# Kernel optimization log

Measured on AMD Instinct MI355X. Metric: run time of the kernel, lower is better.

## Reference

```python
import jax, jax.numpy as jnp
import numpy as np

N, E, D, H = 100000, 800000, 128, 4
DK = D // H
SCALE = 1.0 / np.sqrt(D)  # keep logits tame with random weights
EPS = 1e-5


def _layernorm(x, g, b):
    mu = jnp.mean(x, axis=-1, keepdims=True)
    var = jnp.mean(jnp.square(x - mu), axis=-1, keepdims=True)
    return (x - mu) * jax.lax.rsqrt(var + EPS) * g + b


def setup_inputs() -> dict:
    key = jax.random.key(0)
    ks = jax.random.split(key, 14)
    inp = {
        'h': jax.random.normal(ks[0], (N, D), jnp.float32),
        'e_ij': jax.random.normal(ks[1], (E, D), jnp.float32),
        'W1': jax.random.normal(ks[2], (D, D), jnp.float32) * SCALE,
        'W2': jax.random.normal(ks[3], (D, D), jnp.float32) * SCALE,
        'W3': jax.random.normal(ks[4], (D, D), jnp.float32) * SCALE,
        'W4': jax.random.normal(ks[5], (D, D), jnp.float32) * SCALE,
        'W5': jax.random.normal(ks[6], (D, D), jnp.float32) * SCALE,
        'W6': jax.random.normal(ks[7], (D, D), jnp.float32) * SCALE,
        'ln_gamma': jnp.ones((D,), jnp.float32),
        'ln_beta': jnp.zeros((D,), jnp.float32),
        'mlp_w1': jax.random.normal(ks[8], (D, 2 * D), jnp.float32) * SCALE,
        'mlp_w2': jax.random.normal(ks[9], (2 * D, D), jnp.float32) * (1.0 / np.sqrt(2 * D)),
        'src': jax.random.randint(ks[10], (E,), 0, N, jnp.int32),
        'dst': jax.random.randint(ks[11], (E,), 0, N, jnp.int32),
    }
    return inp


def reference(h, e_ij, W1, W2, W3, W4, W5, W6, ln_gamma, ln_beta, mlp_w1, mlp_w2, src, dst):
    u = (h @ W1).reshape(N, H, DK)      # src-side query
    v = (h @ W2).reshape(N, H, DK)      # dst-side
    x3 = (e_ij @ W3).reshape(E, H, DK)
    # m = v[dst] + x_ij ; attn = u[src] * m (elementwise per head/channel)
    m = v[dst] + x3                      # [E,H,DK]
    attn = (u[src] * m) / np.sqrt(DK)    # [E,H,DK]
    # edge_softmax: segment softmax over incoming edges of each dst node
    amax = jax.ops.segment_max(attn, dst, num_segments=N)   # [N,H,DK]
    ex = jnp.exp(attn - amax[dst])
    denom = jax.ops.segment_sum(ex, dst, num_segments=N)    # [N,H,DK]
    alpha = ex / denom[dst]
    k = (h @ W4).reshape(N, H, DK)
    x5 = (e_ij @ W5).reshape(E, H, DK)
    m2 = k[dst] + x5                     # [E,H,DK]
    agg = jax.ops.segment_sum(alpha * m2, dst, num_segments=N).reshape(N, D)
    h1 = h @ W6 + agg
    h1 = _layernorm(h1, ln_gamma, ln_beta)
    mlp_out = jax.nn.relu(h1 @ mlp_w1) @ mlp_w2
    h2 = _layernorm(h1 + mlp_out, ln_gamma, ln_beta)  # same LayerNorm params reused
    return h2
```

## Files before the change

### kernel.cpp

```cpp
#include <hip/hip_runtime.h>
#include <hip/hip_bf16.h>

#define N_NODES 100000
#define N_EDGES 800000

typedef __attribute__((ext_vector_type(8))) short short8v;
typedef __attribute__((ext_vector_type(4))) float f32x4;

__device__ __forceinline__ unsigned short f2bf(float f) {
    __hip_bfloat16 b = __float2bfloat16(f);
    return *(unsigned short*)&b;
}
__device__ __forceinline__ float bf2f(unsigned short u) {
    return __uint_as_float((unsigned)u << 16);
}
__device__ __forceinline__ unsigned pack2(float lo, float hi) {
    return (unsigned)f2bf(lo) | ((unsigned)f2bf(hi) << 16);
}

__device__ __forceinline__ void gload_lds16(const void* g, void* l) {
    __builtin_amdgcn_global_load_lds(
        (const __attribute__((address_space(1))) unsigned int*)g,
        (__attribute__((address_space(3))) unsigned int*)l,
        16, 0, 0);
}

__device__ __forceinline__ int xcd_swizzle(int orig, int q, int r) {
    int xcd = orig & 7, loc = orig >> 3;
    return (xcd < r ? xcd * (q + 1) : r * (q + 1) + (xcd - r) * q) + loc;
}

__global__ __launch_bounds__(256) void hist_dst(
    const int* __restrict__ dst, int* __restrict__ counts)
{
    int e = blockIdx.x * 256 + threadIdx.x;
    if (e < N_EDGES) atomicAdd(&counts[dst[e]], 1);
}

__global__ __launch_bounds__(256) void scan_p1(
    const int* __restrict__ in, int* __restrict__ partials, int n)
{
    __shared__ int ws[4];
    int t = threadIdx.x, lane = t & 63, wv = t >> 6;
    int base = blockIdx.x * 1024;
    int s = 0;
#pragma unroll
    for (int i = 0; i < 4; ++i) {
        int idx = base + i * 256 + t;
        s += (idx < n) ? in[idx] : 0;
    }
#pragma unroll
    for (int off = 1; off < 64; off <<= 1) s += __shfl_xor(s, off);
    if (lane == 0) ws[wv] = s;
    __syncthreads();
    if (t == 0) partials[blockIdx.x] = ws[0] + ws[1] + ws[2] + ws[3];
}

__global__ __launch_bounds__(64) void scan_p2(
    int* __restrict__ partials, int nb, int* __restrict__ total_out)
{
    int lane = threadIdx.x;
    int carry = 0;
    for (int base = 0; base < nb; base += 64) {
        int idx = base + lane;
        int v = (idx < nb) ? partials[idx] : 0;
        int s = v;
#pragma unroll
        for (int off = 1; off < 64; off <<= 1) {
            int w = __shfl_up(s, off);
            if (lane >= off) s += w;
        }
        if (idx < nb) partials[idx] = s - v + carry;
        carry += __shfl(s, 63);
    }
    if (lane == 0) *total_out = carry;
}

__global__ __launch_bounds__(256) void scan_p3(
    const int* __restrict__ in, int* __restrict__ out, int* __restrict__ cursor,
    const int* __restrict__ partials, int n)
{
    __shared__ int ws[4];
    __shared__ int wpre[4];
    __shared__ int s_tot;
    int t = threadIdx.x, lane = t & 63, wv = t >> 6;
    int base = blockIdx.x * 1024;
    int carry = partials[blockIdx.x];
    for (int sub = 0; sub < 4; ++sub) {
        int idx = base + sub * 256 + t;
        int v = (idx < n) ? in[idx] : 0;
        int s = v;
#pragma unroll
        for (int off = 1; off < 64; off <<= 1) {
            int w = __shfl_up(s, off);
            if (lane >= off) s += w;
        }
        if (lane == 63) ws[wv] = s;
        __syncthreads();
        if (t == 0) {
            int a = 0;
#pragma unroll
            for (int i = 0; i < 4; ++i) { wpre[i] = a; a += ws[i]; }
            s_tot = a;
        }
        __syncthreads();
        int excl = s - v + wpre[wv] + carry;
        if (idx < n) { out[idx] = excl; if (cursor) cursor[idx] = excl; }
        carry += s_tot;
        __syncthreads();
    }
}

__global__ __launch_bounds__(256) void scatter_edges(
    const int* __restrict__ dst, const int* __restrict__ src,
    int* __restrict__ cursor,
    int* __restrict__ edge_ord, int* __restrict__ src_ord,
    int* __restrict__ dst_ord)
{
    int e = blockIdx.x * 256 + threadIdx.x;
    if (e < N_EDGES) {
        int d = dst[e];
        int pos = atomicAdd(&cursor[d], 1);
        edge_ord[pos] = e;
        src_ord[pos] = src[e];
        dst_ord[pos] = d;
    }
}

__global__ __launch_bounds__(256) void calc_npieces(
    const int* __restrict__ offsets, int* __restrict__ npieces)
{
    int n = blockIdx.x * 256 + threadIdx.x;
    if (n < N_NODES) {
        int b = offsets[n], e = offsets[n + 1];
        npieces[n] = (e > b) ? (((e - 1) >> 6) - (b >> 6) + 1) : 0;
    }
}

__global__ __launch_bounds__(256) void prep_weights(
    const float* __restrict__ W1, const float* __restrict__ W2,
    const float* __restrict__ W3, const float* __restrict__ W4,
    const float* __restrict__ W5, const float* __restrict__ W6,
    const float* __restrict__ mw1, const float* __restrict__ mw2,
    unsigned short* __restrict__ w3t, unsigned short* __restrict__ w5t,
    unsigned short* __restrict__ wcatt,
    unsigned short* __restrict__ mw1t, unsigned short* __restrict__ mw2t)
{
    int bid = blockIdx.x;
    if (bid < 64) {
        int t = bid * 256 + threadIdx.x;
        int r = t >> 7, c = t & 127;
        w3t[c * 128 + r] = f2bf(W3[t]);
        w5t[c * 128 + r] = f2bf(W5[t]);
    } else if (bid < 320) {
        int t = (bid - 64) * 256 + threadIdx.x;
        int n = t >> 7, k = t & 127;
        const float* Wm = (n < 128) ? W1 : (n < 256) ? W2 : (n < 384) ? W4 : W6;
        wcatt[t] = f2bf(Wm[k * 128 + (n & 127)]);
    } else {
        int t = (bid - 320) * 256 + threadIdx.x;
        if (t < 32768) {
            int n = t >> 7, k = t & 127;
            mw1t[t] = f2bf(mw1[k * 256 + n]);
        } else {
            int s = t - 32768;
            int n = s >> 8, k = s & 255;
            mw2t[s] = f2bf(mw2[k * 128 + n]);
        }
    }
}

__global__ __launch_bounds__(256) void gemm_node(
    const float* __restrict__ A, const unsigned short* __restrict__ Bt,
    unsigned short* __restrict__ uvkb, float* __restrict__ hw6f)
{
    const int t = threadIdx.x;
    const int lane = t & 63, wv = t >> 6;
    const int l15 = lane & 15, kg = lane >> 4;
    const int m0 = blockIdx.x * 64;
    const int n0 = blockIdx.y * 128;
    const int M = N_NODES, K = 128;

    int arow = m0 + wv * 16 + l15;
    int arow_c = arow < M ? arow : M - 1;
    const float* ap = A + (size_t)arow_c * K + kg * 8;

    f32x4 acc[8];
#pragma unroll
    for (int nt = 0; nt < 8; ++nt) acc[nt] = (f32x4){0.f, 0.f, 0.f, 0.f};

    for (int ko = 0; ko < K; ko += 32) {
        float4 f0 = *(const float4*)(ap + ko);
        float4 f1 = *(const float4*)(ap + ko + 4);
        short8v af;
        af[0] = (short)f2bf(f0.x); af[1] = (short)f2bf(f0.y);
        af[2] = (short)f2bf(f0.z); af[3] = (short)f2bf(f0.w);
        af[4] = (short)f2bf(f1.x); af[5] = (short)f2bf(f1.y);
        af[6] = (short)f2bf(f1.z); af[7] = (short)f2bf(f1.w);
#pragma unroll
        for (int nt = 0; nt < 8; ++nt) {
            short8v bf = *(const short8v*)(Bt + (size_t)(n0 + nt * 16 + l15) * K + ko + kg * 8);
            acc[nt] = __builtin_amdgcn_mfma_f32_16x16x32_bf16(af, bf, acc[nt], 0, 0, 0);
        }
    }
#pragma unroll
    for (int nt = 0; nt < 8; ++nt) {
#pragma unroll
        for (int r = 0; r < 4; ++r) {
            int row = m0 + wv * 16 + kg * 4 + r;
            if (row < M) {
                int col = n0 + nt * 16 + l15;
                float vfl = acc[nt][r];
                if (n0 < 384) uvkb[(size_t)row * 384 + col] = f2bf(vfl);
                else          hw6f[(size_t)row * 128 + col - 384] = vfl;
            }
        }
    }
}

__global__ __launch_bounds__(256, 4) void edge_agg(
    const float* __restrict__ e_ij,
    const unsigned short* __restrict__ w3t, const unsigned short* __restrict__ w5t,
    const unsigned short* __restrict__ uvkb,
    const int* __restrict__ edge_ord, const int* __restrict__ src_ord,
    const int* __restrict__ dst_ord,
    const int* __restrict__ offsets, const int* __restrict__ ppos,
    float* __restrict__ dpart, float* __restrict__ apart)
{
    __shared__ __align__(16) float e_s[64 * 128];
    __shared__ int s_eid[64], s_src[64], s_dst[64];
    __shared__ int s_sb[64], s_se[64], s_pi[64];
    __shared__ int s_nseg;

    const int t  = threadIdx.x;
    const int lane = t & 63, wv = t >> 6;
    const int l15 = lane & 15, kg = lane >> 4;
    const int cb = wv * 32 + 2 * l15;
    const float inv = 0.17677669529663687f;

    const int nwg = N_EDGES / 64;
    const int bswz = xcd_swizzle((int)blockIdx.x, nwg >> 3, nwg & 7);
    const int e0 = bswz * 64;

    if (t < 64) {
        s_eid[t] = edge_ord[e0 + t];
        s_src[t] = src_ord[e0 + t];
        int d = dst_ord[e0 + t];
        s_dst[t] = d;
        int dprev = __shfl_up(d, 1);
        bool bnd = (t == 0) || (d != dprev);
        unsigned long long mask = __ballot(bnd);
        int sid = __popcll(mask & ((1ull << t) - 1ull));
        if (bnd) {
            s_sb[sid] = t;
            s_pi[sid] = ppos[d] + bswz - (offsets[d] >> 6);
            if (t > 0) s_se[sid - 1] = t;
        }
        if (t == 63) {
            int ns = __popcll(mask);
            s_se[ns - 1] = 64;
            s_nseg = ns;
        }
    }
    __syncthreads();

#pragma unroll
    for (int i = 0; i < 8; ++i) {
        int c = i * 256 + t;
        int row = c >> 5, j = c & 31;
        int js = j ^ (row & 7);
        const float* g = e_ij + (size_t)s_eid[row] * 128 + js * 4;
        void* l = (void*)((char*)(&e_s[0]) + (size_t)i * 4096 + (size_t)wv * 1024);
        gload_lds16(g, l);
    }
    __syncthreads();

    unsigned short* eb = (unsigned short*)&e_s[0];
    {
        const int crow = t >> 2, q = t & 3;
        float4 fr[8];
#pragma unroll
        for (int i = 0; i < 8; ++i) {
            int j = (q * 8 + i) ^ (crow & 7);
            fr[i] = *(const float4*)(&e_s[crow * 128 + j * 4]);
        }
        __syncthreads();
#pragma unroll
        for (int i = 0; i < 4; ++i) {
            short8v pk;
            pk[0] = (short)f2bf(fr[2 * i].x);     pk[1] = (short)f2bf(fr[2 * i].y);
            pk[2] = (short)f2bf(fr[2 * i].z);     pk[3] = (short)f2bf(fr[2 * i].w);
            pk[4] = (short)f2bf(fr[2 * i + 1].x); pk[5] = (short)f2bf(fr[2 * i + 1].y);
            pk[6] = (short)f2bf(fr[2 * i + 1].z); pk[7] = (short)f2bf(fr[2 * i + 1].w);
            int c = (q * 4 + i) ^ (crow & 15);
            *(short8v*)(eb + crow * 128 + c * 8) = pk;
        }
    }
    __syncthreads();

    const int nseg = __builtin_amdgcn_readfirstlane(s_nseg);

    f32x4 a3[4][2], a5[4][2];
#pragma unroll
    for (int m = 0; m < 4; ++m) {
        a3[m][0] = (f32x4){0.f, 0.f, 0.f, 0.f};
        a3[m][1] = (f32x4){0.f, 0.f, 0.f, 0.f};
        a5[m][0] = (f32x4){0.f, 0.f, 0.f, 0.f};
        a5[m][1] = (f32x4){0.f, 0.f, 0.f, 0.f};
    }
    {
        const unsigned short* b3p0 = w3t + (size_t)(cb + 0) * 128 + kg * 8;
        const unsigned short* b3p1 = w3t + (size_t)(cb + 1) * 128 + kg * 8;
        const unsigned short* b5p0 = w5t + (size_t)(cb + 0) * 128 + kg * 8;
        const unsigned short* b5p1 = w5t + (size_t)(cb + 1) * 128 + kg * 8;
#pragma unroll
        for (int kidx = 0; kidx < 4; ++kidx) {
            const int ko = kidx * 32;
            short8v b30 = *(const short8v*)(b3p0 + ko);
            short8v b31 = *(const short8v*)(b3p1 + ko);
            short8v b50 = *(const short8v*)(b5p0 + ko);
            short8v b51 = *(const short8v*)(b5p1 + ko);
#pragma unroll
            for (int m = 0; m < 4; ++m) {
                const int row = m * 16 + l15;
                short8v af = *(const short8v*)(eb + row * 128 + (((kidx << 2) | kg) ^ l15) * 8);
                a3[m][0] = __builtin_amdgcn_mfma_f32_16x16x32_bf16(af, b30, a3[m][0], 0, 0, 0);
                a3[m][1] = __builtin_amdgcn_mfma_f32_16x16x32_bf16(af, b31, a3[m][1], 0, 0, 0);
                a5[m][0] = __builtin_amdgcn_mfma_f32_16x16x32_bf16(af, b50, a5[m][0], 0, 0, 0);
                a5[m][1] = __builtin_amdgcn_mfma_f32_16x16x32_bf16(af, b51, a5[m][1], 0, 0, 0);
            }
        }
    }

#pragma unroll
    for (int m = 0; m < 4; ++m) {
#pragma unroll
        for (int r = 0; r < 4; ++r) {
            int le = m * 16 + kg * 4 + r;
            int d  = s_dst[le];
            int sv = s_src[le];
            unsigned upk = *(const unsigned*)&uvkb[(size_t)sv * 384 + cb];
            unsigned vpk = *(const unsigned*)&uvkb[(size_t)d * 384 + 128 + cb];
            float u0 = bf2f((unsigned short)(upk & 0xffffu));
            float u1 = bf2f((unsigned short)(upk >> 16));
            float v0 = bf2f((unsigned short)(vpk & 0xffffu));
            float v1 = bf2f((unsigned short)(vpk >> 16));
            float at0 = u0 * (v0 + a3[m][0][r]) * inv;
            float at1 = u1 * (v1 + a3[m][1][r]) * inv;
            float ex0 = __expf(fminf(at0, 80.f));
            float ex1 = __expf(fminf(at1, 80.f));
            a3[m][0][r] = ex0;
            a3[m][1][r] = ex1;
            a5[m][0][r] = ex0 * a5[m][0][r];
            a5[m][1][r] = ex1 * a5[m][1][r];
        }
    }

    for (int sg = 0; sg < nseg; ++sg) {
        const int b  = __builtin_amdgcn_readfirstlane(s_sb[sg]);
        const int e2 = __builtin_amdgcn_readfirstlane(s_se[sg]);
        const int pi = __builtin_amdgcn_readfirstlane(s_pi[sg]);
        float d0 = 0.f, d1 = 0.f, g0 = 0.f, g1 = 0.f;
#pragma unroll
        for (int m = 0; m < 4; ++m) {
            if (b < m * 16 + 16 && e2 > m * 16) {
#pragma unroll
                for (int r = 0; r < 4; ++r) {
                    int slot = m * 16 + kg * 4 + r;
                    bool in = (slot >= b) && (slot < e2);
                    d0 += in ? a3[m][0][r] : 0.f;
                    d1 += in ? a3[m][1][r] : 0.f;
                    g0 += in ? a5[m][0][r] : 0.f;
                    g1 += in ? a5[m][1][r] : 0.f;
                }
            }
        }
        d0 += __shfl_xor(d0, 16); d0 += __shfl_xor(d0, 32);
        d1 += __shfl_xor(d1, 16); d1 += __shfl_xor(d1, 32);
        g0 += __shfl_xor(g0, 16); g0 += __shfl_xor(g0, 32);
        g1 += __shfl_xor(g1, 16); g1 += __shfl_xor(g1, 32);
        if (kg == 0) {
            *(float2*)&dpart[(size_t)pi * 128 + cb] = make_float2(d0, d1);
            *(float2*)&apart[(size_t)pi * 128 + cb] = make_float2(g0, g1);
        }
    }
}

__global__ __launch_bounds__(256, 2) void node_tail(
    const float* __restrict__ hw6f, const unsigned short* __restrict__ uvkb,
    const float* __restrict__ dpart, const float* __restrict__ apart,
    const int* __restrict__ ppos,
    const unsigned short* __restrict__ mw1t, const unsigned short* __restrict__ mw2t,
    const float* __restrict__ gamma, const float* __restrict__ beta,
    float* __restrict__ out)
{
    __shared__ __align__(16) float h1f[64 * 132];
    __shared__ __align__(16) unsigned short hid[64 * 264];

    const int t = threadIdx.x;
    const int lane = t & 63, wv = t >> 6;
    const int l15 = lane & 15, kg = lane >> 4;
    const int nb = blockIdx.x * 64;

    for (int i = 0; i < 16; ++i) {
        int row = wv * 16 + i;
        int n = nb + row;
        int nc = n < N_NODES ? n : N_NODES - 1;
        int p0 = ppos[nc], p1 = ppos[nc + 1];
        float de0 = 0.f, de1 = 0.f, g0 = 0.f, g1 = 0.f;
        for (int j = p0; j < p1; ++j) {
            float2 dv = *(const float2*)&dpart[(size_t)j * 128 + lane * 2];
            float2 av = *(const float2*)&apart[(size_t)j * 128 + lane * 2];
            de0 += dv.x; de1 += dv.y;
            g0  += av.x; g1  += av.y;
        }
        unsigned kpk = *(const unsigned*)&uvkb[(size_t)nc * 384 + 256 + lane * 2];
        float k0 = bf2f((unsigned short)(kpk & 0xffffu));
        float k1 = bf2f((unsigned short)(kpk >> 16));
        float2 hw = *(const float2*)&hw6f[(size_t)nc * 128 + lane * 2];
        float x0 = hw.x + (de0 > 0.f ? k0 + g0 / de0 : 0.f);
        float x1 = hw.y + (de1 > 0.f ? k1 + g1 / de1 : 0.f);
        float s = x0 + x1;
#pragma unroll
        for (int off = 1; off < 64; off <<= 1) s += __shfl_xor(s, off);
        float mu = s * (1.f / 128.f);
        float d0 = x0 - mu, d1 = x1 - mu;
        float ss = d0 * d0 + d1 * d1;
#pragma unroll
        for (int off = 1; off < 64; off <<= 1) ss += __shfl_xor(ss, off);
        float rs = rsqrtf(ss * (1.f / 128.f) + 1e-5f);
        float2 g = *(const float2*)&gamma[lane * 2];
        float2 b = *(const float2*)&beta[lane * 2];
        h1f[row * 132 + lane * 2]     = d0 * rs * g.x + b.x;
        h1f[row * 132 + lane * 2 + 1] = d1 * rs * g.y + b.y;
    }
    __syncthreads();

    {
        const int arow = wv * 16 + l15;
        f32x4 acc[16];
#pragma unroll
        for (int nt = 0; nt < 16; ++nt) acc[nt] = (f32x4){0.f, 0.f, 0.f, 0.f};
#pragma unroll
        for (int kidx = 0; kidx < 4; ++kidx) {
            const int ko = kidx * 32;
            const float* rp = &h1f[arow * 132 + ko + kg * 8];
            float4 f0 = *(const float4*)rp;
            float4 f1 = *(const float4*)(rp + 4);
            short8v af;
            af[0] = (short)f2bf(f0.x); af[1] = (short)f2bf(f0.y);
            af[2] = (short)f2bf(f0.z); af[3] = (short)f2bf(f0.w);
            af[4] = (short)f2bf(f1.x); af[5] = (short)f2bf(f1.y);
            af[6] = (short)f2bf(f1.z); af[7] = (short)f2bf(f1.w);
#pragma unroll
            for (int nt = 0; nt < 16; ++nt) {
                short8v bf = *(const short8v*)(mw1t + (size_t)(nt * 16 + l15) * 128 + ko + kg * 8);
                acc[nt] = __builtin_amdgcn_mfma_f32_16x16x32_bf16(af, bf, acc[nt], 0, 0, 0);
            }
        }
#pragma unroll
        for (int nt = 0; nt < 16; ++nt) {
#pragma unroll
            for (int r = 0; r < 4; ++r) {
                int row = wv * 16 + kg * 4 + r;
                int col = nt * 16 + l15;
                hid[row * 264 + col] = f2bf(fmaxf(acc[nt][r], 0.f));
            }
        }
    }
    __syncthreads();

    {
        const int arow = wv * 16 + l15;
        f32x4 acc[8];
#pragma unroll
        for (int nt = 0; nt < 8; ++nt) acc[nt] = (f32x4){0.f, 0.f, 0.f, 0.f};
#pragma unroll
        for (int kidx = 0; kidx < 8; ++kidx) {
            const int ko = kidx * 32;
            short8v af = *(const short8v*)&hid[arow * 264 + ko + kg * 8];
#pragma unroll
            for (int nt = 0; nt < 8; ++nt) {
                short8v bf = *(const short8v*)(mw2t + (size_t)(nt * 16 + l15) * 256 + ko + kg * 8);
                acc[nt] = __builtin_amdgcn_mfma_f32_16x16x32_bf16(af, bf, acc[nt], 0, 0, 0);
            }
        }
        float gv[8], bv[8];
#pragma unroll
        for (int nt = 0; nt < 8; ++nt) {
            gv[nt] = gamma[nt * 16 + l15];
            bv[nt] = beta[nt * 16 + l15];
        }
#pragma unroll
        for (int r = 0; r < 4; ++r) {
            int lrow = wv * 16 + kg * 4 + r;
            int grow = nb + lrow;
            float x[8];
            float s = 0.f;
#pragma unroll
            for (int nt = 0; nt < 8; ++nt) {
                x[nt] = acc[nt][r] + h1f[lrow * 132 + nt * 16 + l15];
                s += x[nt];
            }
#pragma unroll
            for (int off = 1; off < 16; off <<= 1) s += __shfl_xor(s, off);
            float mu = s * (1.f / 128.f);
            float ss = 0.f;
#pragma unroll
            for (int nt = 0; nt < 8; ++nt) {
                float d = x[nt] - mu;
                ss += d * d;
            }
#pragma unroll
            for (int off = 1; off < 16; off <<= 1) ss += __shfl_xor(ss, off);
            float rsv = rsqrtf(ss * (1.f / 128.f) + 1e-5f);
            if (grow < N_NODES) {
#pragma unroll
                for (int nt = 0; nt < 8; ++nt)
                    out[(size_t)grow * 128 + nt * 16 + l15] =
                        (x[nt] - mu) * rsv * gv[nt] + bv[nt];
            }
        }
    }
}

extern "C" void kernel_launch(void* const* d_in, const int* in_sizes, int n_in,
                              void* d_out, int out_size, void* d_ws, size_t ws_size,
                              hipStream_t stream)
{
    const float* h    = (const float*)d_in[0];
    const float* e_ij = (const float*)d_in[1];
    const float* W1   = (const float*)d_in[2];
    const float* W2   = (const float*)d_in[3];
    const float* W3   = (const float*)d_in[4];
    const float* W4   = (const float*)d_in[5];
    const float* W5   = (const float*)d_in[6];
    const float* W6   = (const float*)d_in[7];
    const float* ln_g = (const float*)d_in[8];
    const float* ln_b = (const float*)d_in[9];
    const float* mw1  = (const float*)d_in[10];
    const float* mw2  = (const float*)d_in[11];
    const int*   src  = (const int*)d_in[12];
    const int*   dst  = (const int*)d_in[13];
    float* out = (float*)d_out;

    float* ws = (float*)d_ws;
    float* hw6f  = ws;
    float* dpart = ws + 25600000;
    float* apart = ws + 40100000;
    unsigned short* uvkb  = (unsigned short*)(ws + 54600000);
    unsigned short* w3t   = (unsigned short*)(ws + 93000000);
    unsigned short* w5t   = w3t + 16384;
    unsigned short* wcatt = w5t + 16384;
    unsigned short* mw1t  = wcatt + 65536;
    unsigned short* mw2t  = mw1t + 32768;
    int* ibase    = (int*)(ws + 93100000);
    int* counts   = ibase;
    int* offsets  = ibase + 100000;
    int* cursor   = ibase + 200001;
    int* npieces  = ibase + 300001;
    int* ppos     = ibase + 400001;
    int* partials = ibase + 500102;
    int* edge_ord = ibase + 500230;
    int* src_ord  = edge_ord + N_EDGES;
    int* dst_ord  = src_ord + N_EDGES;

    dim3 blk(256);
    hipMemsetAsync(counts, 0, N_NODES * sizeof(int), stream);

    hist_dst<<<N_EDGES / 256, blk, 0, stream>>>(dst, counts);
    scan_p1<<<98, blk, 0, stream>>>(counts, partials, N_NODES);
    scan_p2<<<1, 64, 0, stream>>>(partials, 98, offsets + N_NODES);
    scan_p3<<<98, blk, 0, stream>>>(counts, offsets, cursor, partials, N_NODES);
    scatter_edges<<<N_EDGES / 256, blk, 0, stream>>>(dst, src, cursor,
                                                     edge_ord, src_ord, dst_ord);
    calc_npieces<<<391, blk, 0, stream>>>(offsets, npieces);
    scan_p1<<<98, blk, 0, stream>>>(npieces, partials, N_NODES);
    scan_p2<<<1, 64, 0, stream>>>(partials, 98, ppos + N_NODES);
    scan_p3<<<98, blk, 0, stream>>>(npieces, ppos, (int*)nullptr, partials, N_NODES);

    prep_weights<<<576, blk, 0, stream>>>(W1, W2, W3, W4, W5, W6, mw1, mw2,
                                          w3t, w5t, wcatt, mw1t, mw2t);

    gemm_node<<<dim3(1563, 4), blk, 0, stream>>>(h, wcatt, uvkb, hw6f);

    edge_agg<<<N_EDGES / 64, blk, 0, stream>>>(e_ij, w3t, w5t, uvkb,
                                               edge_ord, src_ord, dst_ord,
                                               offsets, ppos, dpart, apart);

    node_tail<<<1563, blk, 0, stream>>>(hw6f, uvkb, dpart, apart, ppos,
                                        mw1t, mw2t, ln_g, ln_b, out);
}
```

Measured before the change: 672.7 us.

## Split node tail into per-node finalize kernel and separate MLP kernel

The fused node_tail kernel, which reduced edge partials, applied the first LayerNorm and ran the MLP with the second LayerNorm, is split in two. node_finalize assigns one wavefront per node and writes h1 in fp32 and bf16 to workspace. mlp_tail reads the bf16 h1 as its MFMA A operand and the fp32 h1 as the residual, and asks for higher occupancy. The aim is more parallelism in the serial, latency-bound partial reduction, which looped over 16 nodes per wave. The cost is an extra launch and an extra round trip of h1 through global memory.

```diff
diff --git a/kernel.cpp b/kernel.cpp
--- a/kernel.cpp
+++ b/kernel.cpp
@@ -386,72 +386,73 @@
     }
 }
 
-__global__ __launch_bounds__(256, 2) void node_tail(
+__global__ __launch_bounds__(256) void node_finalize(
     const float* __restrict__ hw6f, const unsigned short* __restrict__ uvkb,
     const float* __restrict__ dpart, const float* __restrict__ apart,
     const int* __restrict__ ppos,
+    const float* __restrict__ gamma, const float* __restrict__ beta,
+    float* __restrict__ h1, unsigned short* __restrict__ h1b)
+{
+    int n = blockIdx.x * 4 + (threadIdx.x >> 6);
+    int lane = threadIdx.x & 63;
+    int p0 = ppos[n], p1 = ppos[n + 1];
+    float de0 = 0.f, de1 = 0.f, g0 = 0.f, g1 = 0.f;
+    for (int j = p0; j < p1; ++j) {
+        float2 dv = *(const float2*)&dpart[(size_t)j * 128 + lane * 2];
+        float2 av = *(const float2*)&apart[(size_t)j * 128 + lane * 2];
+        de0 += dv.x; de1 += dv.y;
+        g0  += av.x; g1  += av.y;
+    }
+    unsigned kpk = *(const unsigned*)&uvkb[(size_t)n * 384 + 256 + lane * 2];
+    float k0 = bf2f((unsigned short)(kpk & 0xffffu));
+    float k1 = bf2f((unsigned short)(kpk >> 16));
+    float2 hw = *(const float2*)&hw6f[(size_t)n * 128 + lane * 2];
+    float x0 = hw.x + (de0 > 0.f ? k0 + g0 / de0 : 0.f);
+    float x1 = hw.y + (de1 > 0.f ? k1 + g1 / de1 : 0.f);
+    float s = x0 + x1;
+#pragma unroll
+    for (int off = 1; off < 64; off <<= 1) s += __shfl_xor(s, off);
+    float mu = s * (1.f / 128.f);
+    float d0 = x0 - mu, d1 = x1 - mu;
+    float ss = d0 * d0 + d1 * d1;
+#pragma unroll
+    for (int off = 1; off < 64; off <<= 1) ss += __shfl_xor(ss, off);
+    float rs = rsqrtf(ss * (1.f / 128.f) + 1e-5f);
+    float2 g = *(const float2*)&gamma[lane * 2];
+    float2 b = *(const float2*)&beta[lane * 2];
+    float o0 = d0 * rs * g.x + b.x;
+    float o1 = d1 * rs * g.y + b.y;
+    size_t base = (size_t)n * 128 + lane * 2;
+    *(float2*)&h1[base] = make_float2(o0, o1);
+    *(unsigned*)&h1b[base] = pack2(o0, o1);
+}
+
+__global__ __launch_bounds__(256, 4) void mlp_tail(
+    const unsigned short* __restrict__ A,
+    const float* __restrict__ res,
     const unsigned short* __restrict__ mw1t, const unsigned short* __restrict__ mw2t,
     const float* __restrict__ gamma, const float* __restrict__ beta,
     float* __restrict__ out)
 {
-    __shared__ __align__(16) float h1f[64 * 132];
     __shared__ __align__(16) unsigned short hid[64 * 264];
 
     const int t = threadIdx.x;
     const int lane = t & 63, wv = t >> 6;
     const int l15 = lane & 15, kg = lane >> 4;
-    const int nb = blockIdx.x * 64;
-
-    for (int i = 0; i < 16; ++i) {
-        int row = wv * 16 + i;
-        int n = nb + row;
-        int nc = n < N_NODES ? n : N_NODES - 1;
-        int p0 = ppos[nc], p1 = ppos[nc + 1];
-        float de0 = 0.f, de1 = 0.f, g0 = 0.f, g1 = 0.f;
-        for (int j = p0; j < p1; ++j) {
-            float2 dv = *(const float2*)&dpart[(size_t)j * 128 + lane * 2];
-            float2 av = *(const float2*)&apart[(size_t)j * 128 + lane * 2];
-            de0 += dv.x; de1 += dv.y;
-            g0  += av.x; g1  += av.y;
-        }
-        unsigned kpk = *(const unsigned*)&uvkb[(size_t)nc * 384 + 256 + lane * 2];
-        float k0 = bf2f((unsigned short)(kpk & 0xffffu));
-        float k1 = bf2f((unsigned short)(kpk >> 16));
-        float2 hw = *(const float2*)&hw6f[(size_t)nc * 128 + lane * 2];
-        float x0 = hw.x + (de0 > 0.f ? k0 + g0 / de0 : 0.f);
-        float x1 = hw.y + (de1 > 0.f ? k1 + g1 / de1 : 0.f);
-        float s = x0 + x1;
-#pragma unroll
-        for (int off = 1; off < 64; off <<= 1) s += __shfl_xor(s, off);
-        float mu = s * (1.f / 128.f);
-        float d0 = x0 - mu, d1 = x1 - mu;
-        float ss = d0 * d0 + d1 * d1;
-#pragma unroll
-        for (int off = 1; off < 64; off <<= 1) ss += __shfl_xor(ss, off);
-        float rs = rsqrtf(ss * (1.f / 128.f) + 1e-5f);
-        float2 g = *(const float2*)&gamma[lane * 2];
-        float2 b = *(const float2*)&beta[lane * 2];
-        h1f[row * 132 + lane * 2]     = d0 * rs * g.x + b.x;
-        h1f[row * 132 + lane * 2 + 1] = d1 * rs * g.y + b.y;
-    }
-    __syncthreads();
+    const int m0 = blockIdx.x * 64;
+    const int M = N_NODES;
 
     {
-        const int arow = wv * 16 + l15;
+        int arow = m0 + wv * 16 + l15;
+        int arow_c = arow < M ? arow : M - 1;
+        const unsigned short* ap = A + (size_t)arow_c * 128 + kg * 8;
         f32x4 acc[16];
 #pragma unroll
         for (int nt = 0; nt < 16; ++nt) acc[nt] = (f32x4){0.f, 0.f, 0.f, 0.f};
 #pragma unroll
         for (int kidx = 0; kidx < 4; ++kidx) {
             const int ko = kidx * 32;
-            const float* rp = &h1f[arow * 132 + ko + kg * 8];
-            float4 f0 = *(const float4*)rp;
-            float4 f1 = *(const float4*)(rp + 4);
-            short8v af;
-            af[0] = (short)f2bf(f0.x); af[1] = (short)f2bf(f0.y);
-            af[2] = (short)f2bf(f0.z); af[3] = (short)f2bf(f0.w);
-            af[4] = (short)f2bf(f1.x); af[5] = (short)f2bf(f1.y);
-            af[6] = (short)f2bf(f1.z); af[7] = (short)f2bf(f1.w);
+            short8v af = *(const short8v*)(ap + ko);
 #pragma unroll
             for (int nt = 0; nt < 16; ++nt) {
                 short8v bf = *(const short8v*)(mw1t + (size_t)(nt * 16 + l15) * 128 + ko + kg * 8);
@@ -471,14 +472,14 @@
     __syncthreads();
 
     {
-        const int arow = wv * 16 + l15;
+        const int lrow = wv * 16 + l15;
         f32x4 acc[8];
 #pragma unroll
         for (int nt = 0; nt < 8; ++nt) acc[nt] = (f32x4){0.f, 0.f, 0.f, 0.f};
 #pragma unroll
         for (int kidx = 0; kidx < 8; ++kidx) {
             const int ko = kidx * 32;
-            short8v af = *(const short8v*)&hid[arow * 264 + ko + kg * 8];
+            short8v af = *(const short8v*)&hid[lrow * 264 + ko + kg * 8];
 #pragma unroll
             for (int nt = 0; nt < 8; ++nt) {
                 short8v bf = *(const short8v*)(mw2t + (size_t)(nt * 16 + l15) * 256 + ko + kg * 8);
@@ -493,13 +494,13 @@
         }
 #pragma unroll
         for (int r = 0; r < 4; ++r) {
-            int lrow = wv * 16 + kg * 4 + r;
-            int grow = nb + lrow;
+            int row = m0 + wv * 16 + kg * 4 + r;
+            int rc = row < M ? row : M - 1;
             float x[8];
             float s = 0.f;
 #pragma unroll
             for (int nt = 0; nt < 8; ++nt) {
-                x[nt] = acc[nt][r] + h1f[lrow * 132 + nt * 16 + l15];
+                x[nt] = acc[nt][r] + res[(size_t)rc * 128 + nt * 16 + l15];
                 s += x[nt];
             }
 #pragma unroll
@@ -514,10 +515,10 @@
 #pragma unroll
             for (int off = 1; off < 16; off <<= 1) ss += __shfl_xor(ss, off);
             float rsv = rsqrtf(ss * (1.f / 128.f) + 1e-5f);
-            if (grow < N_NODES) {
+            if (row < M) {
 #pragma unroll
                 for (int nt = 0; nt < 8; ++nt)
-                    out[(size_t)grow * 128 + nt * 16 + l15] =
+                    out[(size_t)row * 128 + nt * 16 + l15] =
                         (x[nt] - mu) * rsv * gv[nt] + bv[nt];
             }
         }
@@ -546,9 +547,11 @@
 
     float* ws = (float*)d_ws;
     float* hw6f  = ws;
+    float* h1    = ws + 12800000;
     float* dpart = ws + 25600000;
     float* apart = ws + 40100000;
     unsigned short* uvkb  = (unsigned short*)(ws + 54600000);
+    unsigned short* h1b   = (unsigned short*)(ws + 73800000);
     unsigned short* w3t   = (unsigned short*)(ws + 93000000);
     unsigned short* w5t   = w3t + 16384;
     unsigned short* wcatt = w5t + 16384;
@@ -588,6 +591,8 @@
                                                edge_ord, src_ord, dst_ord,
                                                offsets, ppos, dpart, apart);
 
-    node_tail<<<1563, blk, 0, stream>>>(hw6f, uvkb, dpart, apart, ppos,
-                                        mw1t, mw2t, ln_g, ln_b, out);
-}
+    node_finalize<<<N_NODES / 4, blk, 0, stream>>>(hw6f, uvkb, dpart, apart, ppos,
+                                                   ln_g, ln_b, h1, h1b);
+
+    mlp_tail<<<1563, blk, 0, stream>>>(h1b, h1, mw1t, mw2t, ln_g, ln_b, out);
+}
```

Result: faster. 612.7 us (median of 2 runs) (-8.9%).
